# Performance work log

Hardware: AMD Instinct MI355X
Metric: run time of the kernel (lower is better)

## Reference

```python
import jax, jax.numpy as jnp
import numpy as np

ALPHA = 0.2  # LeakyReLU negative slope used throughout
NEG = -9e15


def _leaky(x, a=ALPHA):
    return jnp.where(x >= 0, x, a * x)


def _gat_layer(h, adj, W, a, concat):
    # h: [N, Fin], W: [Fin, Fout], a: [2*Fout, 1]
    Wh = h @ W                                   # [N, Fout]
    d = W.shape[-1]
    e = _leaky(Wh @ a[:d] + (Wh @ a[d:]).T)      # [N, N]
    att = jax.nn.softmax(jnp.where(adj > 0, e, NEG), axis=1)
    out = att @ Wh                               # [N, Fout]
    return jax.nn.elu(out) if concat else out


def setup_inputs() -> dict:
    key = jax.random.key(0)
    ks = jax.random.split(key, 24)
    N, F, H, D1, O1 = 4096, 512, 4, 256, 64
    x = jax.random.normal(ks[0], (N, F), dtype=jnp.float32)
    adj = jax.random.bernoulli(ks[1], 0.02, (N, N))
    adj = (adj | adj.T | jnp.eye(N, dtype=bool)).astype(jnp.float32)
    observation = jax.random.randint(ks[2], (1, N), 0, 2, dtype=jnp.int32)
    s_mat = jax.random.uniform(ks[3], (N, N), dtype=jnp.float32)
    theta = jax.random.uniform(ks[4], (1, F), dtype=jnp.float32)
    g = lambda k, s, sc: (jax.random.normal(k, s, dtype=jnp.float32) * sc)
    return {
        'x': x, 'adj': adj, 'observation': observation, 's_mat': s_mat,
        'theta': theta,
        'Wh0': g(ks[5], (H, F, D1), 0.05), 'ah0': g(ks[6], (H, 2 * D1, 1), 0.05),
        'Wh1': g(ks[7], (H, D1, D1), 0.05), 'ah1': g(ks[8], (H, 2 * D1, 1), 0.05),
        'Wo0': g(ks[9], (H * D1, O1), 0.05), 'ao0': g(ks[10], (2 * O1, 1), 0.05),
        'Wo1': g(ks[11], (O1, 1), 0.2), 'ao1': g(ks[12], (2, 1), 0.2),
        'dW': g(ks[13], (2, 10), 0.5), 'dW0': g(ks[14], (1, 10), 0.5),
        'dW1': g(ks[15], (10, 20), 0.5), 'dW01': g(ks[16], (1, 20), 0.5),
        'dW2': g(ks[17], (20, 10), 0.5), 'dW02': g(ks[18], (1, 10), 0.5),
        'dV': g(ks[19], (10, 1), 0.5), 'dV0': g(ks[20], (1, 1), 0.5),
    }


def reference(x, adj, observation, s_mat, theta, Wh0, ah0, Wh1, ah1,
              Wo0, ao0, Wo1, ao1, dW, dW0, dW1, dW01, dW2, dW02, dV, dV0):
    # mergeState: add theta to rows in the seed set (observation[0] == 1)
    seed = (observation[0] == 1).astype(x.dtype)[:, None]  # [N,1]
    h_in = x + seed * theta

    # multi-head 2-layer attention stacks (concat=True -> elu inside)
    def head(W0, a0, W1, a1):
        h = _gat_layer(h_in, adj, W0, a0, True)
        return _gat_layer(h, adj, W1, a1, True)

    hh = jax.vmap(head)(Wh0, ah0, Wh1, ah1)                 # [H, N, D1]
    hcat = jnp.transpose(hh, (1, 0, 2)).reshape(h_in.shape[0], -1)  # [N, H*D1]

    # output attention stack (concat=False), then elu (GAT.forward)
    h = _gat_layer(hcat, adj, Wo0, ao0, False)
    h = _gat_layer(h, adj, Wo1, ao1, False)
    h_ = jax.nn.elu(h)                                      # [N, 1]

    # GAT_degree v2: degreeNN over [h_, degree]
    d_v = s_mat.sum(axis=1, keepdims=True)                  # [N, 1]
    x_ = jnp.concatenate([h_, d_v], axis=1)                 # [N, 2]
    h0 = _leaky(x_ @ dW + dW0)
    h1 = _leaky(h0 @ dW1 + dW01)
    h2 = _leaky(h1 @ dW2 + dW02)
    return _leaky(h2 @ dV + dV0)                            # [N, 1]
```

## Files before the change

kernel.cpp:

```cpp
#include <hip/hip_runtime.h>
#include <hip/hip_bf16.h>
#include <hip/hip_fp16.h>
#include <math.h>

#define MAXDEG 512

typedef short v8s __attribute__((ext_vector_type(8)));
typedef float v4f __attribute__((ext_vector_type(4)));
typedef _Float16 h2 __attribute__((ext_vector_type(2)));

__device__ __forceinline__ float blockReduceSum(float v) {
    __shared__ float sh[8];
    int lane = threadIdx.x & 63, w = threadIdx.x >> 6;
    for (int o = 32; o > 0; o >>= 1) v += __shfl_down(v, o);
    __syncthreads();
    if (lane == 0) sh[w] = v;
    __syncthreads();
    if (w == 0) {
        int nw = (blockDim.x + 63) >> 6;
        v = (lane < nw) ? sh[lane] : 0.f;
        for (int o = 4; o > 0; o >>= 1) v += __shfl_down(v, o);
        if (lane == 0) sh[0] = v;
    }
    __syncthreads();
    return sh[0];
}

__device__ __forceinline__ float blockReduceMax(float v) {
    __shared__ float sh[8];
    int lane = threadIdx.x & 63, w = threadIdx.x >> 6;
    for (int o = 32; o > 0; o >>= 1) v = fmaxf(v, __shfl_down(v, o));
    __syncthreads();
    if (lane == 0) sh[w] = v;
    __syncthreads();
    if (w == 0) {
        int nw = (blockDim.x + 63) >> 6;
        v = (lane < nw) ? sh[lane] : -3.4e38f;
        for (int o = 4; o > 0; o >>= 1) v = fmaxf(v, __shfl_down(v, o));
        if (lane == 0) sh[0] = v;
    }
    __syncthreads();
    return sh[0];
}

__device__ __forceinline__ float leaky(float x) { return x >= 0.f ? x : 0.2f * x; }


__global__ void fused_pre(const float* __restrict__ adj, const float* __restrict__ s,
                          int* __restrict__ colIdx, int* __restrict__ deg,
                          float* __restrict__ dv,
                          const float* __restrict__ x, const int* __restrict__ obs,
                          const float* __restrict__ theta,
                          const float* __restrict__ Wh0, const float* __restrict__ Wh1,
                          const float* __restrict__ Wo0,
                          __half* __restrict__ hin, __half* __restrict__ Wh0t,
                          __half* __restrict__ Wh1t, __half* __restrict__ Wo0t,
                          float* __restrict__ elerZ, int elerN, int N) {
    if (blockIdx.x < 4096) {
        int row = blockIdx.x;
        __shared__ int cnt;
        if (threadIdx.x == 0) cnt = 0;
        __syncthreads();
        const float4* ar = (const float4*)(adj + (size_t)row * N);
        const float4* sr = (const float4*)(s + (size_t)row * N);
        int* outp = colIdx + (size_t)row * MAXDEG;
        float psum = 0.f;
        const int n4 = N >> 2;
        for (int j4 = threadIdx.x; j4 < n4; j4 += blockDim.x) {
            float4 a4 = ar[j4];
            float4 s4 = sr[j4];
            psum += (s4.x + s4.y) + (s4.z + s4.w);
            int jb = j4 << 2;
            if (a4.x > 0.f) { int p = atomicAdd(&cnt, 1); if (p < MAXDEG) outp[p] = jb; }
            if (a4.y > 0.f) { int p = atomicAdd(&cnt, 1); if (p < MAXDEG) outp[p] = jb + 1; }
            if (a4.z > 0.f) { int p = atomicAdd(&cnt, 1); if (p < MAXDEG) outp[p] = jb + 2; }
            if (a4.w > 0.f) { int p = atomicAdd(&cnt, 1); if (p < MAXDEG) outp[p] = jb + 3; }
        }
        psum = blockReduceSum(psum);
        __syncthreads();
        if (threadIdx.x == 0) {
            deg[row] = cnt < MAXDEG ? cnt : MAXDEG;
            dv[row] = psum;
        }
        return;
    }
    const int n0 = 4096 * 512;
    const int n1 = 4 * 512 * 256;
    const int n2 = 4 * 256 * 256;
    const int n3 = 1024 * 64;
    int i = (blockIdx.x - 4096) * 256 + threadIdx.x;
    if (i < n0) {
        int n = i >> 9, f = i & 511;
        float v = x[i];
        if (obs[n] == 1) v += theta[f];
        hin[i] = __float2half(v);
    } else if (i < n0 + n1) {
        int t = i - n0;
        int b = t / (512 * 256), r = t % (512 * 256);
        int mm = r >> 9, kk = r & 511;
        Wh0t[t] = __float2half(Wh0[b * 512 * 256 + kk * 256 + mm]);
    } else if (i < n0 + n1 + n2) {
        int t = i - n0 - n1;
        int b = t >> 16, r = t & 65535;
        int mm = r >> 8, kk = r & 255;
        Wh1t[t] = __float2half(Wh1[b * 65536 + kk * 256 + mm]);
    } else if (i < n0 + n1 + n2 + n3) {
        int t = i - n0 - n1 - n2;
        int mm = t >> 10, kk = t & 1023;
        Wo0t[t] = __float2half(Wo0[kk * 64 + mm]);
    } else if (i < n0 + n1 + n2 + n3 + elerN) {
        elerZ[i - n0 - n1 - n2 - n3] = 0.f;
    }
}

__global__ __launch_bounds__(256) void gemm_mfma128(
    const __half* __restrict__ A, const __half* __restrict__ Bt,
    __half* __restrict__ C, int N, int K, int M,
    size_t sA, size_t sB, size_t sC,
    const float* __restrict__ aVec, size_t aStride,
    float* __restrict__ el, float* __restrict__ er) {
    int b = blockIdx.z;
    const unsigned short* Ag = (const unsigned short*)(A + (size_t)b * sA);
    const unsigned short* Bg = (const unsigned short*)(Bt + (size_t)b * sB);
    __half* Cg = C + (size_t)b * sC;
    const float* av = aVec + (size_t)b * aStride;

    __shared__ __align__(16) unsigned short As[128][40];
    __shared__ __align__(16) unsigned short Bs[128][40];

    const int tid = threadIdx.x;
    const int wave = tid >> 6, lane = tid & 63;
    const int wm = wave >> 1, wn = wave & 1;
    const int row0 = blockIdx.y * 128, col0 = blockIdx.x * 128;
    const int lr = tid >> 2;
    const int lo = (tid & 3) * 8;
    const int m = lane & 15, quad = lane >> 4;

    v4f acc[4][4];
    #pragma unroll
    for (int i = 0; i < 4; i++)
        #pragma unroll
        for (int c = 0; c < 4; c++) acc[i][c] = (v4f)(0.f);

    for (int k0 = 0; k0 < K; k0 += 32) {
        *(int4*)(&As[lr][lo]) =
            *(const int4*)(Ag + (size_t)(row0 + lr) * K + k0 + lo);
        *(int4*)(&As[lr + 64][lo]) =
            *(const int4*)(Ag + (size_t)(row0 + 64 + lr) * K + k0 + lo);
        *(int4*)(&Bs[lr][lo]) =
            *(const int4*)(Bg + (size_t)(col0 + lr) * K + k0 + lo);
        *(int4*)(&Bs[lr + 64][lo]) =
            *(const int4*)(Bg + (size_t)(col0 + 64 + lr) * K + k0 + lo);
        __syncthreads();
        v8s af[4], bfv[4];
        #pragma unroll
        for (int i = 0; i < 4; i++)
            af[i] = *(const v8s*)(&As[wm * 64 + i * 16 + m][quad * 8]);
        #pragma unroll
        for (int c = 0; c < 4; c++)
            bfv[c] = *(const v8s*)(&Bs[wn * 64 + c * 16 + m][quad * 8]);
        #pragma unroll
        for (int i = 0; i < 4; i++)
            #pragma unroll
            for (int c = 0; c < 4; c++)
                acc[i][c] = __builtin_amdgcn_mfma_f32_16x16x32_f16(
                    af[i], bfv[c], acc[i][c], 0, 0, 0);
        __syncthreads();
    }
    #pragma unroll
    for (int i = 0; i < 4; i++)
        #pragma unroll
        for (int c = 0; c < 4; c++)
            #pragma unroll
            for (int r = 0; r < 4; r++) {
                int row = row0 + wm * 64 + i * 16 + quad * 4 + r;
                int col = col0 + wn * 64 + c * 16 + m;
                Cg[(size_t)row * M + col] = __float2half(acc[i][c][r]);
            }
    float ael[4], aer[4];
    #pragma unroll
    for (int c = 0; c < 4; c++) {
        ael[c] = av[col0 + wn * 64 + c * 16 + m];
        aer[c] = av[M + col0 + wn * 64 + c * 16 + m];
    }
    #pragma unroll
    for (int i = 0; i < 4; i++)
        #pragma unroll
        for (int r = 0; r < 4; r++) {
            float pel = 0.f, per_ = 0.f;
            #pragma unroll
            for (int c = 0; c < 4; c++) {
                pel += acc[i][c][r] * ael[c];
                per_ += acc[i][c][r] * aer[c];
            }
            #pragma unroll
            for (int off = 1; off < 16; off <<= 1) {
                pel += __shfl_xor(pel, off);
                per_ += __shfl_xor(per_, off);
            }
            if (m == 0) {
                int row = row0 + wm * 64 + i * 16 + quad * 4 + r;
                atomicAdd(&el[(size_t)b * N + row], pel);
                atomicAdd(&er[(size_t)b * N + row], per_);
            }
        }
}

__global__ __launch_bounds__(256) void gemm_mfma64(
    const __half* __restrict__ A, const __half* __restrict__ Bt,
    __half* __restrict__ C, int N, int K, int M,
    size_t sA, size_t sB, size_t sC,
    const float* __restrict__ aVec, size_t aStride,
    float* __restrict__ el, float* __restrict__ er) {
    int b = blockIdx.z;
    const unsigned short* Ag = (const unsigned short*)(A + (size_t)b * sA);
    const unsigned short* Bg = (const unsigned short*)(Bt + (size_t)b * sB);
    __half* Cg = C + (size_t)b * sC;
    const float* av = aVec + (size_t)b * aStride;

    __shared__ __align__(16) unsigned short As[64][40];
    __shared__ __align__(16) unsigned short Bs[64][40];

    const int tid = threadIdx.x;
    const int wave = tid >> 6, lane = tid & 63;
    const int row0 = blockIdx.y * 64, col0 = blockIdx.x * 64;
    const int sRow = tid >> 2;
    const int sOff = (tid & 3) * 8;
    const int m = lane & 15, quad = lane >> 4;

    v4f acc[4];
    #pragma unroll
    for (int c = 0; c < 4; c++) acc[c] = (v4f)(0.f);

    for (int k0 = 0; k0 < K; k0 += 32) {
        *(int4*)(&As[sRow][sOff]) =
            *(const int4*)(Ag + (size_t)(row0 + sRow) * K + k0 + sOff);
        *(int4*)(&Bs[sRow][sOff]) =
            *(const int4*)(Bg + (size_t)(col0 + sRow) * K + k0 + sOff);
        __syncthreads();
        v8s af = *(const v8s*)(&As[wave * 16 + m][quad * 8]);
        #pragma unroll
        for (int c = 0; c < 4; c++) {
            v8s bfv = *(const v8s*)(&Bs[c * 16 + m][quad * 8]);
            acc[c] = __builtin_amdgcn_mfma_f32_16x16x32_f16(af, bfv, acc[c], 0, 0, 0);
        }
        __syncthreads();
    }
    #pragma unroll
    for (int c = 0; c < 4; c++)
        #pragma unroll
        for (int r = 0; r < 4; r++) {
            int row = row0 + wave * 16 + quad * 4 + r;
            int col = col0 + c * 16 + m;
            Cg[(size_t)row * M + col] = __float2half(acc[c][r]);
        }
    float ael[4], aer[4];
    #pragma unroll
    for (int c = 0; c < 4; c++) {
        ael[c] = av[col0 + c * 16 + m];
        aer[c] = av[M + col0 + c * 16 + m];
    }
    #pragma unroll
    for (int r = 0; r < 4; r++) {
        float pel = 0.f, per_ = 0.f;
        #pragma unroll
        for (int c = 0; c < 4; c++) {
            pel += acc[c][r] * ael[c];
            per_ += acc[c][r] * aer[c];
        }
        #pragma unroll
        for (int off = 1; off < 16; off <<= 1) {
            pel += __shfl_xor(pel, off);
            per_ += __shfl_xor(per_, off);
        }
        if (m == 0) {
            int row = row0 + wave * 16 + quad * 4 + r;
            atomicAdd(&el[(size_t)b * N + row], pel);
            atomicAdd(&er[(size_t)b * N + row], per_);
        }
    }
}

template<int D, int ACT, int HEADS, int FUSE>
__global__ __launch_bounds__(256) void attn_vec(
    const __half* __restrict__ Wh, const float* __restrict__ el,
    const float* __restrict__ er, const int* __restrict__ colIdx,
    const int* __restrict__ deg, __half* __restrict__ out,
    int N, size_t sWh, size_t sOut, int outRowStride,
    const float* __restrict__ wo1, const float* __restrict__ ao1,
    float* __restrict__ o2wh, float* __restrict__ el4, float* __restrict__ er4) {
    constexpr int LPN = D / 8;
    constexpr int SUBS = 64 / LPN;
    constexpr int PER_WAVE = SUBS * 4;
    constexpr int PAD = 4 * PER_WAVE;

    int b, row;
    if (HEADS == 4) {
        int blk = blockIdx.x;
        b = (blk & 7) >> 1;
        row = ((blk >> 3) << 1) | (blk & 1);
    } else {
        b = 0;
        row = blockIdx.x;
    }
    const int tid = threadIdx.x;
    const __half* whb = Wh + (size_t)b * sWh;
    const float* erb = er + (size_t)b * N;
    const float eln = el[(size_t)b * N + row];
    const int dc = deg[row];
    const int dcp = (dc + PAD - 1) & ~(PAD - 1);
    const int* ci = colIdx + (size_t)row * MAXDEG;

    __shared__ __align__(16) float2 spc[MAXDEG];
    __shared__ __align__(16) float redc[4 * D];

    float mx = -3.4e38f;
    for (int k = tid; k < dc; k += 256) {
        int j = ci[k];
        float s = eln + erb[j];
        s = fmaxf(s, 0.2f * s);
        spc[k] = make_float2(s, __int_as_float(j * (D * 2)));
        mx = fmaxf(mx, s);
    }
    for (int k = dc + tid; k < dcp; k += 256)
        spc[k] = make_float2(__int_as_float(0), __int_as_float(0));
    mx = blockReduceMax(mx);
    float l = 0.f;
    for (int k = tid; k < dc; k += 256) {
        float p = __expf(spc[k].x - mx);
        l += p;
        unsigned int pu = __half_as_ushort(__float2half(p));
        spc[k].x = __int_as_float(pu | (pu << 16));
    }
    l = blockReduceSum(l);
    const float inv = 1.f / l;

    const int wave = tid >> 6, lane = tid & 63;
    const int sub = lane / LPN;
    const int dl = (lane % LPN) * 8;
    const char* wp = (const char*)(whb + dl);

    union HU { unsigned int u; h2 h; };
    union R4 { uint4 u; h2 h[4]; };

    h2 a0[4], a1[4];
    #pragma unroll
    for (int i = 0; i < 4; i++) { a0[i] = (h2)(_Float16)0; a1[i] = (h2)(_Float16)0; }

    for (int k = wave * PER_WAVE + sub * 4; k < dcp; k += PAD) {
        float4 pA = *(const float4*)(&spc[k]);
        float4 pB = *(const float4*)(&spc[k + 2]);
        R4 r0, r1, r2, r3;
        r0.u = *(const uint4*)(wp + __float_as_int(pA.y));
        r1.u = *(const uint4*)(wp + __float_as_int(pA.w));
        r2.u = *(const uint4*)(wp + __float_as_int(pB.y));
        r3.u = *(const uint4*)(wp + __float_as_int(pB.w));
        HU p0, p1, p2, p3;
        p0.u = __float_as_int(pA.x);
        p1.u = __float_as_int(pA.z);
        p2.u = __float_as_int(pB.x);
        p3.u = __float_as_int(pB.z);
        #pragma unroll
        for (int i = 0; i < 4; i++) {
            a0[i] += p0.h * r0.h[i];
            a1[i] += p2.h * r2.h[i];
        }
        #pragma unroll
        for (int i = 0; i < 4; i++) {
            a0[i] += p1.h * r1.h[i];
            a1[i] += p3.h * r3.h[i];
        }
    }
    #pragma unroll
    for (int i = 0; i < 4; i++) a0[i] += a1[i];
    #pragma unroll
    for (int off = LPN; off < 64; off <<= 1)
        #pragma unroll
        for (int i = 0; i < 4; i++) {
            HU t, s;
            t.h = a0[i];
            s.u = __shfl_xor((int)t.u, off);
            a0[i] += s.h;
        }
    __syncthreads();
    if (sub == 0)
        #pragma unroll
        for (int i = 0; i < 4; i++) {
            redc[wave * D + dl + 2 * i]     = (float)a0[i][0];
            redc[wave * D + dl + 2 * i + 1] = (float)a0[i][1];
        }
    __syncthreads();
    if (FUSE) {
        if (tid < 64) {
            float vv = (redc[tid] + redc[D + tid] + redc[2 * D + tid] + redc[3 * D + tid]) * inv;
            float t = vv * wo1[tid];
            #pragma unroll
            for (int o = 32; o > 0; o >>= 1) t += __shfl_down(t, o);
            if (tid == 0) {
                o2wh[row] = t;
                el4[row] = t * ao1[0];
                er4[row] = t * ao1[1];
            }
        }
        return;
    }
    if (tid < D) {
        float v = (redc[tid] + redc[D + tid] + redc[2 * D + tid] + redc[3 * D + tid]) * inv;
        if (ACT == 1) v = (v > 0.f) ? v : expm1f(v);
        out[(size_t)b * sOut + (size_t)row * outRowStride + tid] = __float2half(v);
    }
}

__global__ void attn_d1_deg(const float* __restrict__ o2wh, const float* __restrict__ el,
                            const float* __restrict__ er, const int* __restrict__ colIdx,
                            const int* __restrict__ deg, const float* __restrict__ dv,
                            const float* __restrict__ dW, const float* __restrict__ dW0,
                            const float* __restrict__ dW1, const float* __restrict__ dW01,
                            const float* __restrict__ dW2, const float* __restrict__ dW02,
                            const float* __restrict__ dV, const float* __restrict__ dV0,
                            float* __restrict__ out, int N) {
    int row = blockIdx.x, tid = threadIdx.x;
    const float eln = el[row];
    const int dc = deg[row];
    const int* ci = colIdx + (size_t)row * MAXDEG;
    __shared__ float sp[MAXDEG];
    __shared__ int sc[MAXDEG];
    float mx = -3.4e38f;
    for (int k = tid; k < dc; k += blockDim.x) {
        int j = ci[k];
        sc[k] = j;
        float s = eln + er[j];
        s = fmaxf(s, 0.2f * s);
        sp[k] = s;
        mx = fmaxf(mx, s);
    }
    mx = blockReduceMax(mx);
    float l = 0.f, acc = 0.f;
    for (int k = tid; k < dc; k += blockDim.x) {
        float p = __expf(sp[k] - mx);
        l += p;
        acc += p * o2wh[sc[k]];
    }
    l = blockReduceSum(l);
    acc = blockReduceSum(acc);
    if (tid == 0) {
        float h = acc / l;
        h = (h > 0.f) ? h : expm1f(h);
        float d = dv[row];
        float t0[10], t1[20], t2[10];
        #pragma unroll
        for (int i = 0; i < 10; i++)
            t0[i] = leaky(h * dW[i] + d * dW[10 + i] + dW0[i]);
        #pragma unroll
        for (int j = 0; j < 20; j++) {
            float s = dW01[j];
            #pragma unroll
            for (int i = 0; i < 10; i++) s += t0[i] * dW1[i * 20 + j];
            t1[j] = leaky(s);
        }
        #pragma unroll
        for (int j = 0; j < 10; j++) {
            float s = dW02[j];
            #pragma unroll
            for (int i = 0; i < 20; i++) s += t1[i] * dW2[i * 10 + j];
            t2[j] = leaky(s);
        }
        float o = dV0[0];
        #pragma unroll
        for (int i = 0; i < 10; i++) o += t2[i] * dV[i];
        out[row] = leaky(o);
    }
}

extern "C" void kernel_launch(void* const* d_in, const int* in_sizes, int n_in,
                              void* d_out, int out_size, void* d_ws, size_t ws_size,
                              hipStream_t stream) {
    const int N = 4096, F = 512, H = 4, D1 = 256, O1 = 64;
    const float* x     = (const float*)d_in[0];
    const float* adj   = (const float*)d_in[1];
    const int*   obs   = (const int*)  d_in[2];
    const float* s_mat = (const float*)d_in[3];
    const float* theta = (const float*)d_in[4];
    const float* Wh0   = (const float*)d_in[5];
    const float* ah0   = (const float*)d_in[6];
    const float* Wh1   = (const float*)d_in[7];
    const float* ah1   = (const float*)d_in[8];
    const float* Wo0   = (const float*)d_in[9];
    const float* ao0   = (const float*)d_in[10];
    const float* Wo1   = (const float*)d_in[11];
    const float* ao1   = (const float*)d_in[12];
    const float* dWp   = (const float*)d_in[13];
    const float* dW0p  = (const float*)d_in[14];
    const float* dW1p  = (const float*)d_in[15];
    const float* dW01p = (const float*)d_in[16];
    const float* dW2p  = (const float*)d_in[17];
    const float* dW02p = (const float*)d_in[18];
    const float* dVp   = (const float*)d_in[19];
    const float* dV0p  = (const float*)d_in[20];
    float* outp = (float*)d_out;

    char* ws = (char*)d_ws;
    auto alloc = [&](size_t bytes) {
        char* p = ws;
        ws += (bytes + 255) & ~(size_t)255;
        return p;
    };
    __half* hin  = (__half*)alloc((size_t)N * F * 2);
    __half* whA  = (__half*)alloc((size_t)H * N * D1 * 2);
    __half* hb   = (__half*)alloc((size_t)H * N * D1 * 2);
    __half* hcat = (__half*)alloc((size_t)N * H * D1 * 2);
    __half* o1Wh = (__half*)alloc((size_t)N * O1 * 2);
    float* o2Wh  = (float*)alloc((size_t)N * 4);
    __half* Wh0t = (__half*)alloc((size_t)H * F * D1 * 2);
    __half* Wh1t = (__half*)alloc((size_t)H * D1 * D1 * 2);
    __half* Wo0t = (__half*)alloc((size_t)H * D1 * O1 * 2);
    int elerN = 4 * H * N + 2 * N;
    float* elerZ = (float*)alloc((size_t)elerN * 4);
    float* el1 = elerZ;
    float* er1 = el1 + H * N;
    float* el2 = er1 + H * N;
    float* er2 = el2 + H * N;
    float* el3 = er2 + H * N;
    float* er3 = el3 + N;
    float* el4 = (float*)alloc((size_t)N * 4);
    float* er4 = (float*)alloc((size_t)N * 4);
    float* dv  = (float*)alloc((size_t)N * 4);
    int* colIdx = (int*)alloc((size_t)N * MAXDEG * 4);
    int* deg    = (int*)alloc((size_t)N * 4);

    {
        const int totalPrep = N * F + H * F * D1 + H * D1 * D1 + H * D1 * O1 + elerN;
        const int prepBlocks = (totalPrep + 255) / 256;
        fused_pre<<<4096 + prepBlocks, 256, 0, stream>>>(
            adj, s_mat, colIdx, deg, dv,
            x, obs, theta, Wh0, Wh1, Wo0, hin, Wh0t, Wh1t, Wo0t, elerZ, elerN, N);
    }

    gemm_mfma128<<<dim3(D1 / 128, N / 128, H), 256, 0, stream>>>(
        hin, Wh0t, whA, N, F, D1, 0, (size_t)D1 * F, (size_t)N * D1,
        ah0, (size_t)2 * D1, el1, er1);
    attn_vec<256, 1, 4, 0><<<N * H, 256, 0, stream>>>(
        whA, el1, er1, colIdx, deg, hb,
        N, (size_t)N * D1, (size_t)N * D1, D1,
        nullptr, nullptr, nullptr, nullptr, nullptr);

    gemm_mfma128<<<dim3(D1 / 128, N / 128, H), 256, 0, stream>>>(
        hb, Wh1t, whA, N, D1, D1, (size_t)N * D1, (size_t)D1 * D1, (size_t)N * D1,
        ah1, (size_t)2 * D1, el2, er2);
    attn_vec<256, 1, 4, 0><<<N * H, 256, 0, stream>>>(
        whA, el2, er2, colIdx, deg, hcat,
        N, (size_t)N * D1, (size_t)D1, H * D1,
        nullptr, nullptr, nullptr, nullptr, nullptr);

    gemm_mfma64<<<dim3(O1 / 64, N / 64, 1), 256, 0, stream>>>(
        hcat, Wo0t, o1Wh, N, H * D1, O1, 0, 0, 0,
        ao0, 0, el3, er3);
    attn_vec<64, 0, 1, 1><<<N, 256, 0, stream>>>(
        o1Wh, el3, er3, colIdx, deg, nullptr,
        N, 0, 0, O1,
        Wo1, ao1, o2Wh, el4, er4);

    attn_d1_deg<<<N, 256, 0, stream>>>(o2Wh, el4, er4, colIdx, deg, dv,
        dWp, dW0p, dW1p, dW01p, dW2p, dW02p, dVp, dV0p, outp, N);
}
```

Baseline: 402.4 us.

## Map one attention row per wavefront instead of one per block

The sparse attention aggregation kernel now gives each wavefront its own (head,row) task, so a block handles four rows and the grid shrinks by four. Softmax max and sum become wave shuffles with scores held in registers, which removes the block-wide reductions, the __syncthreads barriers and the shared-memory cross-wave reduction buffer. Outputs are written as packed 16-byte stores. The trade-off is less parallelism per row (one wave walks the whole neighbour list) and a different block-to-head mapping that may change cache locality for the gathered Wh rows.

```diff
diff --git a/kernel.cpp b/kernel.cpp
--- a/kernel.cpp
+++ b/kernel.cpp
@@ -292,50 +292,62 @@
     constexpr int LPN = D / 8;
     constexpr int SUBS = 64 / LPN;
     constexpr int PER_WAVE = SUBS * 4;
-    constexpr int PAD = 4 * PER_WAVE;
-
+
+    const int tid = threadIdx.x;
+    const int wave = tid >> 6, lane = tid & 63;
+    const int task = blockIdx.x * 4 + wave;
     int b, row;
-    if (HEADS == 4) {
-        int blk = blockIdx.x;
-        b = (blk & 7) >> 1;
-        row = ((blk >> 3) << 1) | (blk & 1);
-    } else {
-        b = 0;
-        row = blockIdx.x;
-    }
-    const int tid = threadIdx.x;
+    if (HEADS == 4) { b = task >> 12; row = task & 4095; }
+    else            { b = 0;          row = task; }
+
     const __half* whb = Wh + (size_t)b * sWh;
     const float* erb = er + (size_t)b * N;
     const float eln = el[(size_t)b * N + row];
     const int dc = deg[row];
-    const int dcp = (dc + PAD - 1) & ~(PAD - 1);
+    const int dcp = (dc + PER_WAVE - 1) & ~(PER_WAVE - 1);
     const int* ci = colIdx + (size_t)row * MAXDEG;
 
-    __shared__ __align__(16) float2 spc[MAXDEG];
-    __shared__ __align__(16) float redc[4 * D];
-
+    __shared__ __align__(16) float2 spc[4][MAXDEG];
+    float2* sp = spc[wave];
+
+    float sreg[8];
+    int jreg[8];
     float mx = -3.4e38f;
-    for (int k = tid; k < dc; k += 256) {
-        int j = ci[k];
-        float s = eln + erb[j];
-        s = fmaxf(s, 0.2f * s);
-        spc[k] = make_float2(s, __int_as_float(j * (D * 2)));
-        mx = fmaxf(mx, s);
-    }
-    for (int k = dc + tid; k < dcp; k += 256)
-        spc[k] = make_float2(__int_as_float(0), __int_as_float(0));
-    mx = blockReduceMax(mx);
+    #pragma unroll
+    for (int s8 = 0; s8 < 8; s8++) {
+        int k = s8 * 64 + lane;
+        if (k < dc) {
+            int j = ci[k];
+            float s = eln + erb[j];
+            s = fmaxf(s, 0.2f * s);
+            sreg[s8] = s;
+            jreg[s8] = j * (D * 2);
+            mx = fmaxf(mx, s);
+        }
+    }
+    #pragma unroll
+    for (int off = 1; off < 64; off <<= 1) mx = fmaxf(mx, __shfl_xor(mx, off));
+
     float l = 0.f;
-    for (int k = tid; k < dc; k += 256) {
-        float p = __expf(spc[k].x - mx);
-        l += p;
-        unsigned int pu = __half_as_ushort(__float2half(p));
-        spc[k].x = __int_as_float(pu | (pu << 16));
-    }
-    l = blockReduceSum(l);
+    #pragma unroll
+    for (int s8 = 0; s8 < 8; s8++) {
+        int k = s8 * 64 + lane;
+        if (k < dc) {
+            float p = __expf(sreg[s8] - mx);
+            l += p;
+            unsigned int pu = __half_as_ushort(__float2half(p));
+            sp[k] = make_float2(__int_as_float(pu | (pu << 16)),
+                                __int_as_float(jreg[s8]));
+        }
+    }
+    for (int k = dc + lane; k < dcp; k += 64)
+        sp[k] = make_float2(__int_as_float(0), __int_as_float(0));
+    #pragma unroll
+    for (int off = 1; off < 64; off <<= 1) l += __shfl_xor(l, off);
     const float inv = 1.f / l;
 
-    const int wave = tid >> 6, lane = tid & 63;
+    asm volatile("s_waitcnt lgkmcnt(0)" ::: "memory");
+
     const int sub = lane / LPN;
     const int dl = (lane % LPN) * 8;
     const char* wp = (const char*)(whb + dl);
@@ -347,9 +359,9 @@
     #pragma unroll
     for (int i = 0; i < 4; i++) { a0[i] = (h2)(_Float16)0; a1[i] = (h2)(_Float16)0; }
 
-    for (int k = wave * PER_WAVE + sub * 4; k < dcp; k += PAD) {
-        float4 pA = *(const float4*)(&spc[k]);
-        float4 pB = *(const float4*)(&spc[k + 2]);
+    for (int k = sub * 4; k < dcp; k += PER_WAVE) {
+        float4 pA = *(const float4*)(&sp[k]);
+        float4 pB = *(const float4*)(&sp[k + 2]);
         R4 r0, r1, r2, r3;
         r0.u = *(const uint4*)(wp + __float_as_int(pA.y));
         r1.u = *(const uint4*)(wp + __float_as_int(pA.w));
@@ -382,21 +394,18 @@
             s.u = __shfl_xor((int)t.u, off);
             a0[i] += s.h;
         }
-    __syncthreads();
-    if (sub == 0)
-        #pragma unroll
-        for (int i = 0; i < 4; i++) {
-            redc[wave * D + dl + 2 * i]     = (float)a0[i][0];
-            redc[wave * D + dl + 2 * i + 1] = (float)a0[i][1];
-        }
-    __syncthreads();
+
     if (FUSE) {
-        if (tid < 64) {
-            float vv = (redc[tid] + redc[D + tid] + redc[2 * D + tid] + redc[3 * D + tid]) * inv;
-            float t = vv * wo1[tid];
-            #pragma unroll
-            for (int o = 32; o > 0; o >>= 1) t += __shfl_down(t, o);
-            if (tid == 0) {
+        if (sub == 0) {
+            float t = 0.f;
+            #pragma unroll
+            for (int i = 0; i < 4; i++) {
+                t += (float)a0[i][0] * inv * wo1[dl + 2 * i];
+                t += (float)a0[i][1] * inv * wo1[dl + 2 * i + 1];
+            }
+            #pragma unroll
+            for (int off = 1; off < LPN; off <<= 1) t += __shfl_xor(t, off);
+            if (lane == 0) {
                 o2wh[row] = t;
                 el4[row] = t * ao1[0];
                 er4[row] = t * ao1[1];
@@ -404,10 +413,21 @@
         }
         return;
     }
-    if (tid < D) {
-        float v = (redc[tid] + redc[D + tid] + redc[2 * D + tid] + redc[3 * D + tid]) * inv;
-        if (ACT == 1) v = (v > 0.f) ? v : expm1f(v);
-        out[(size_t)b * sOut + (size_t)row * outRowStride + tid] = __float2half(v);
+    if (sub == 0) {
+        __half hv[8];
+        #pragma unroll
+        for (int i = 0; i < 4; i++) {
+            float v0 = (float)a0[i][0] * inv;
+            float v1 = (float)a0[i][1] * inv;
+            if (ACT == 1) {
+                v0 = (v0 > 0.f) ? v0 : expm1f(v0);
+                v1 = (v1 > 0.f) ? v1 : expm1f(v1);
+            }
+            hv[2 * i]     = __float2half(v0);
+            hv[2 * i + 1] = __float2half(v1);
+        }
+        *(uint4*)(out + (size_t)b * sOut + (size_t)row * outRowStride + dl) =
+            *(const uint4*)hv;
     }
 }
 
@@ -539,7 +559,7 @@
     gemm_mfma128<<<dim3(D1 / 128, N / 128, H), 256, 0, stream>>>(
         hin, Wh0t, whA, N, F, D1, 0, (size_t)D1 * F, (size_t)N * D1,
         ah0, (size_t)2 * D1, el1, er1);
-    attn_vec<256, 1, 4, 0><<<N * H, 256, 0, stream>>>(
+    attn_vec<256, 1, 4, 0><<<(N * H) / 4, 256, 0, stream>>>(
         whA, el1, er1, colIdx, deg, hb,
         N, (size_t)N * D1, (size_t)N * D1, D1,
         nullptr, nullptr, nullptr, nullptr, nullptr);
@@ -547,7 +567,7 @@
     gemm_mfma128<<<dim3(D1 / 128, N / 128, H), 256, 0, stream>>>(
         hb, Wh1t, whA, N, D1, D1, (size_t)N * D1, (size_t)D1 * D1, (size_t)N * D1,
         ah1, (size_t)2 * D1, el2, er2);
-    attn_vec<256, 1, 4, 0><<<N * H, 256, 0, stream>>>(
+    attn_vec<256, 1, 4, 0><<<(N * H) / 4, 256, 0, stream>>>(
         whA, el2, er2, colIdx, deg, hcat,
         N, (size_t)N * D1, (size_t)D1, H * D1,
         nullptr, nullptr, nullptr, nullptr, nullptr);
@@ -555,7 +575,7 @@
     gemm_mfma64<<<dim3(O1 / 64, N / 64, 1), 256, 0, stream>>>(
         hcat, Wo0t, o1Wh, N, H * D1, O1, 0, 0, 0,
         ao0, 0, el3, er3);
-    attn_vec<64, 0, 1, 1><<<N, 256, 0, stream>>>(
+    attn_vec<64, 0, 1, 1><<<N / 4, 256, 0, stream>>>(
         o1Wh, el3, er3, colIdx, deg, nullptr,
         N, 0, 0, O1,
         Wo1, ao1, o2Wh, el4, er4);
```

New measurement: 388.5 us. 1.04x faster.
